# Performance work log

Hardware: AMD Instinct MI355X
Metric: run time of the kernel (lower is better)

The kernel has to match this reference:

```python
import jax, jax.numpy as jnp
import numpy as np

B, S, D, H = 4, 1024, 1024, 16
DH = D // H
K_SPARSE = 32
LAMBDA_MAX, ALPHA = 10.0, 5.0
SPARSE_THRESHOLD = 1.0


def setup_inputs() -> dict:
    key = jax.random.key(0)
    ks = jax.random.split(key, 12)
    x = jax.random.normal(ks[0], (B, S, D), dtype=jnp.float32)
    prior_mask = jax.random.bernoulli(ks[1], 0.1, (S, S))
    prior_indices = jax.random.randint(ks[2], (S, K_SPARSE), 0, S)
    prior_index_mask = jax.random.bernoulli(ks[3], 0.9, (S, K_SPARSE))
    prior_index_mask = prior_index_mask.at[:, 0].set(True)  # avoid all-masked rows
    u_prev = jax.random.normal(ks[4], (B, 1), dtype=jnp.float32)
    sc = 1.0 / np.sqrt(D)
    Wq = jax.random.normal(ks[5], (D, D), dtype=jnp.float32) * sc
    Wk = jax.random.normal(ks[6], (D, D), dtype=jnp.float32) * sc
    Wv = jax.random.normal(ks[7], (D, D), dtype=jnp.float32) * sc
    Wo = jax.random.normal(ks[8], (D, D), dtype=jnp.float32) * sc
    bq = jnp.zeros((D,), jnp.float32)
    bk = jnp.zeros((D,), jnp.float32)
    bv = jnp.zeros((D,), jnp.float32)
    bo = jnp.zeros((D,), jnp.float32)
    return {"x": x, "prior_mask": prior_mask, "prior_indices": prior_indices,
            "prior_index_mask": prior_index_mask, "u_prev": u_prev,
            "Wq": Wq, "bq": bq, "Wk": Wk, "bk": bk, "Wv": Wv, "bv": bv,
            "Wo": Wo, "bo": bo}


def reference(x, prior_mask, prior_indices, prior_index_mask, u_prev,
              Wq, bq, Wk, bk, Wv, bv, Wo, bo):
    Bb, Ss, Dd = x.shape
    scale = 1.0 / jnp.sqrt(jnp.asarray(DH, x.dtype))

    def proj(W, b):
        return (x @ W.T + b).reshape(Bb, Ss, H, DH).transpose(0, 2, 1, 3)  # [B,H,S,DH]

    Q, K, V = proj(Wq, bq), proj(Wk, bk), proj(Wv, bv)

    lam = LAMBDA_MAX * jnp.exp(-ALPHA * u_prev.reshape(Bb))  # [B]
    use_sparse = lam >= SPARSE_THRESHOLD                      # [B] bool

    # ---- dense branch: full SDPA with lambda-scaled prior bias ----
    scores = jnp.einsum('bhqd,bhkd->bhqk', Q, K) * scale      # [B,H,S,S]
    prior_bias = jnp.where(prior_mask[:Ss, :Ss], 0.0, -1.0).astype(x.dtype)
    bias = lam[:, None, None, None] * prior_bias[None, None]
    dense_out = jnp.einsum('bhqk,bhkd->bhqd',
                           jax.nn.softmax(scores + bias, axis=-1), V)

    # ---- sparse branch: gather-indexed SDPA over prior_indices ----
    idx = prior_indices[:Ss]                                   # [S,k]
    Kg = K[:, :, idx]                                          # [B,H,S,k,DH]
    Vg = V[:, :, idx]
    s_scores = jnp.einsum('bhsd,bhskd->bhsk', Q, Kg) * scale   # [B,H,S,k]
    s_scores = jnp.where(prior_index_mask[:Ss][None, None], s_scores,
                         jnp.asarray(-jnp.inf, x.dtype))
    sparse_out = jnp.einsum('bhsk,bhskd->bhsd',
                            jax.nn.softmax(s_scores, axis=-1), Vg)

    out = jnp.where(use_sparse[:, None, None, None], sparse_out, dense_out)
    out = out.transpose(0, 2, 1, 3).reshape(Bb, Ss, Dd)
    return out @ Wo.T + bo
```

## Files before the change

### kernel.cpp

```cpp
#include <hip/hip_runtime.h>
#include <hip/hip_bf16.h>
#include <cmath>

#define NB 4
#define NS 1024
#define ND 1024
#define NH 16
#define NDH 64
#define NKSP 32
#define SCALE 0.125f
#define LOG2E 1.44269504f
#define SCALE2 (SCALE * LOG2E)

typedef __attribute__((ext_vector_type(8))) short bf16x8;
typedef __attribute__((ext_vector_type(4))) float f32x4;
typedef unsigned long long u64;

#define AS1 __attribute__((address_space(1)))
#define AS3 __attribute__((address_space(3)))

__device__ __forceinline__ void gl_lds16(const void* g, void* l) {
    __builtin_amdgcn_global_load_lds((const AS1 void*)g, (AS3 void*)l, 16, 0, 0);
}

__device__ __forceinline__ ushort f2bf(float f) {
    union { __hip_bfloat16 h; ushort u; } cv;
    cv.h = __float2bfloat16(f);
    return cv.u;
}
__device__ __forceinline__ float bf2f(ushort u) {
    union { unsigned int i; float f; } cv;
    cv.i = ((unsigned int)u) << 16;
    return cv.f;
}
__device__ __forceinline__ float fexp2(float x) {
    return __builtin_amdgcn_exp2f(x);
}

__global__ __launch_bounds__(256)
void f2bf_multi(const float* __restrict__ x,
                const float* __restrict__ w0, const float* __restrict__ w1,
                const float* __restrict__ w2, const float* __restrict__ w3,
                const int* __restrict__ pm,
                ushort* __restrict__ xo,
                ushort* __restrict__ o0, ushort* __restrict__ o1,
                ushort* __restrict__ o2, ushort* __restrict__ o3,
                u64* __restrict__ bm)
{
    int y = blockIdx.y;
    if (y == 5) {
        int word = blockIdx.x * 4 + (threadIdx.x >> 6);
        int lane = threadIdx.x & 63;
        int row  = word >> 4, wcol = word & 15;
        int v = pm[(size_t)row * NS + wcol * 64 + lane];
        u64 b = __ballot(v != 0);
        if (lane == 0) bm[word] = b;
        return;
    }
    const float* src; ushort* dst; int nblk;
    if (y == 0)      { src = x;  dst = xo; nblk = 4096; }
    else if (y == 1) { src = w0; dst = o0; nblk = 1024; }
    else if (y == 2) { src = w1; dst = o1; nblk = 1024; }
    else if (y == 3) { src = w2; dst = o2; nblk = 1024; }
    else             { src = w3; dst = o3; nblk = 1024; }
    if (blockIdx.x >= (unsigned)nblk) return;
    int i = (blockIdx.x * 256 + threadIdx.x) * 4;
    float4 v = *(const float4*)&src[i];
    ushort4 o;
    o.x = f2bf(v.x); o.y = f2bf(v.y); o.z = f2bf(v.z); o.w = f2bf(v.w);
    *(ushort4*)&dst[i] = o;
}

__global__ __launch_bounds__(256)
void gemm_qkv(const ushort* __restrict__ xb,
              const ushort* __restrict__ Wqb, const ushort* __restrict__ Wkb,
              const ushort* __restrict__ Wvb,
              const float* __restrict__ bq, const float* __restrict__ bk,
              const float* __restrict__ bv,
              ushort* __restrict__ Qo, ushort* __restrict__ Ko,
              ushort* __restrict__ Vo, ushort* __restrict__ Vto)
{
    constexpr int K = ND;
    __shared__ __attribute__((aligned(16))) ushort As[128 * 32];
    __shared__ __attribute__((aligned(16))) ushort Bs[128 * 32];

    const int tid  = threadIdx.x;
    const int lane = tid & 63, w = tid >> 6;
    const int wm = w >> 1, wn = w & 1;
    const int which = blockIdx.x >> 3;
    const int n0 = (blockIdx.x & 7) * 128;
    const int m0 = blockIdx.y * 128;
    const int quad = lane >> 4, l16 = lane & 15;

    const ushort* W = (which == 0) ? Wqb : (which == 1) ? Wkb : Wvb;
    const float* bias = (which == 0) ? bq : (which == 1) ? bk : bv;
    ushort* Out = (which == 0) ? Qo : (which == 1) ? Ko : Vo;

    f32x4 acc[4][4] = {};

    for (int k0 = 0; k0 < K; k0 += 32) {
        __syncthreads();
#pragma unroll
        for (int u = 0; u < 2; ++u) {
            int t0 = u * 256 + w * 64;
            int t  = t0 + lane;
            int row = t >> 2, kc = (t & 3) * 8;
            gl_lds16(xb + (size_t)(m0 + row) * K + k0 + kc, &As[t0 * 8]);
            gl_lds16(W  + (size_t)(n0 + row) * K + k0 + kc, &Bs[t0 * 8]);
        }
        __syncthreads();

        bf16x8 af[4], bfr[4];
#pragma unroll
        for (int mt = 0; mt < 4; ++mt)
            af[mt] = *(const bf16x8*)&As[(wm*64 + mt*16 + l16) * 32 + quad*8];
#pragma unroll
        for (int nt = 0; nt < 4; ++nt)
            bfr[nt] = *(const bf16x8*)&Bs[(wn*64 + nt*16 + l16) * 32 + quad*8];
#pragma unroll
        for (int mt = 0; mt < 4; ++mt)
#pragma unroll
            for (int nt = 0; nt < 4; ++nt)
                acc[mt][nt] = __builtin_amdgcn_mfma_f32_16x16x32_bf16(
                    af[mt], bfr[nt], acc[mt][nt], 0, 0, 0);
    }

#pragma unroll
    for (int nt = 0; nt < 4; ++nt) {
        int n = n0 + wn*64 + nt*16 + l16;
        float bz = bias[n];
        int hh = n >> 6, dh = n & 63;
#pragma unroll
        for (int mt = 0; mt < 4; ++mt) {
#pragma unroll
            for (int rg = 0; rg < 4; ++rg) {
                int m = m0 + wm*64 + mt*16 + quad*4 + rg;
                int b = m >> 10, s = m & (NS - 1);
                ushort val = f2bf(acc[mt][nt][rg] + bz);
                Out[(((size_t)(b*NH + hh))*NS + s)*NDH + dh] = val;
                if (which == 2)
                    Vto[(((size_t)(b*NH + hh))*NDH + dh)*NS + s] = val;
            }
        }
    }
}

__global__ __launch_bounds__(256)
void gemm_out(const ushort* __restrict__ A, const ushort* __restrict__ W,
              const float* __restrict__ bias, float* __restrict__ Cout)
{
    constexpr int K = ND;
    __shared__ __attribute__((aligned(16))) ushort As[64 * 32];
    __shared__ __attribute__((aligned(16))) ushort Bs[128 * 32];

    const int tid  = threadIdx.x;
    const int lane = tid & 63, w = tid >> 6;
    const int wm = w & 1, wn = w >> 1;
    const int m0 = blockIdx.y * 64, n0 = blockIdx.x * 128;
    const int quad = lane >> 4, l16 = lane & 15;

    f32x4 acc[2][4] = {};

    for (int k0 = 0; k0 < K; k0 += 32) {
        __syncthreads();
        {
            int t0 = w * 64;
            int t  = t0 + lane;
            int row = t >> 2, kc = (t & 3) * 8;
            gl_lds16(A + (size_t)(m0 + row) * K + k0 + kc, &As[t0 * 8]);
        }
#pragma unroll
        for (int u = 0; u < 2; ++u) {
            int t0 = u * 256 + w * 64;
            int t  = t0 + lane;
            int row = t >> 2, kc = (t & 3) * 8;
            gl_lds16(W + (size_t)(n0 + row) * K + k0 + kc, &Bs[t0 * 8]);
        }
        __syncthreads();

        bf16x8 af[2], bfr[4];
#pragma unroll
        for (int mt = 0; mt < 2; ++mt)
            af[mt] = *(const bf16x8*)&As[(wm*32 + mt*16 + l16) * 32 + quad*8];
#pragma unroll
        for (int nt = 0; nt < 4; ++nt)
            bfr[nt] = *(const bf16x8*)&Bs[(wn*64 + nt*16 + l16) * 32 + quad*8];
#pragma unroll
        for (int mt = 0; mt < 2; ++mt)
#pragma unroll
            for (int nt = 0; nt < 4; ++nt)
                acc[mt][nt] = __builtin_amdgcn_mfma_f32_16x16x32_bf16(
                    af[mt], bfr[nt], acc[mt][nt], 0, 0, 0);
    }

#pragma unroll
    for (int nt = 0; nt < 4; ++nt) {
        int n = n0 + wn*64 + nt*16 + l16;
        float bz = bias[n];
#pragma unroll
        for (int mt = 0; mt < 2; ++mt) {
#pragma unroll
            for (int rg = 0; rg < 4; ++rg) {
                int m = m0 + wm*32 + mt*16 + quad*4 + rg;
                Cout[(size_t)m * ND + n] = acc[mt][nt][rg] + bz;
            }
        }
    }
}


#define STAGE(BUF, PT)                                                        \
    _Pragma("unroll")                                                         \
    for (int u = 0; u < 4; ++u) {                                             \
        int cb = w * 256 + u * 64;                                            \
        int c  = cb + lane;                                                   \
        int wk2 = c >> 9, c2 = c & 511;                                       \
        int row = c2 >> 3, sub = c2 & 7;                                      \
        const ushort* src = Kh + (((size_t)(((PT) + wk2)*64 + row)) << 6)     \
                               + ((sub ^ (row & 7)) << 3);                    \
        gl_lds16(src, (ushort*)KK + (BUF)*8192 + (size_t)cb * 8);             \
    }

#define LOADKV(KF, VF, BUF, KT)                                               \
    _Pragma("unroll")                                                         \
    for (int nt = 0; nt < 4; ++nt)                                            \
        _Pragma("unroll")                                                     \
        for (int kk = 0; kk < 2; ++kk) {                                      \
            int rowk = nt*16 + l16;                                           \
            int ck = (kk*4 + quad) ^ (l16 & 7);                               \
            KF[nt][kk] = *(const bf16x8*)                                     \
                &((ushort*)KK)[(BUF)*8192 + wk*4096 + rowk*64 + ck*8];        \
            VF[nt][kk] = *(const bf16x8*)                                     \
                &Vth[(size_t)(nt*16 + l16) * NS + (KT)*64 + kk*32 + quad*8];  \
        }

#define STEP(KT, KF, VF)                                                      \
    _Pragma("unroll")                                                         \
    for (int qh = 0; qh < 2; ++qh) {                                          \
        const int qrow = wq*32 + qh*16 + l16;                                 \
        u64 wqm = MW[(KT)*64 + qrow] >> (quad * 4);                           \
        f32x4 s_acc[4] = {};                                                  \
        __builtin_amdgcn_s_setprio(1);                                        \
        _Pragma("unroll")                                                     \
        for (int nt = 0; nt < 4; ++nt)                                        \
            _Pragma("unroll")                                                 \
            for (int kk = 0; kk < 2; ++kk)                                    \
                s_acc[nt] = __builtin_amdgcn_mfma_f32_16x16x32_bf16(          \
                    KF[nt][kk], qf[qh][kk], s_acc[nt], 0, 0, 0);              \
        __builtin_amdgcn_s_setprio(0);                                        \
        _Pragma("unroll")                                                     \
        for (int nt = 0; nt < 4; ++nt) {                                      \
            ushort4 pk;                                                       \
            float p0 = fexp2(fmaf(s_acc[nt][0], SCALE2,                       \
                 ((wqm >> (nt*16 + 0)) & 1ULL) ? 0.f : nlam2));               \
            float p1 = fexp2(fmaf(s_acc[nt][1], SCALE2,                       \
                 ((wqm >> (nt*16 + 1)) & 1ULL) ? 0.f : nlam2));               \
            float p2 = fexp2(fmaf(s_acc[nt][2], SCALE2,                       \
                 ((wqm >> (nt*16 + 2)) & 1ULL) ? 0.f : nlam2));               \
            float p3 = fexp2(fmaf(s_acc[nt][3], SCALE2,                       \
                 ((wqm >> (nt*16 + 3)) & 1ULL) ? 0.f : nlam2));               \
            pk.x = f2bf(p0); pk.y = f2bf(p1);                                 \
            pk.z = f2bf(p2); pk.w = f2bf(p3);                                 \
            *(ushort4*)&Ps[wk][qrow*72 + nt*16 + quad*4] = pk;                \
        }                                                                     \
        bf16x8 pf[2];                                                         \
        _Pragma("unroll")                                                     \
        for (int kk = 0; kk < 2; ++kk)                                        \
            pf[kk] = *(const bf16x8*)&Ps[wk][qrow*72 + kk*32 + quad*8];       \
        __builtin_amdgcn_s_setprio(1);                                        \
        _Pragma("unroll")                                                     \
        for (int kk = 0; kk < 2; ++kk) {                                      \
            l_acc[qh] = __builtin_amdgcn_mfma_f32_16x16x32_bf16(              \
                pf[kk], ones.v, l_acc[qh], 0, 0, 0);                          \
            _Pragma("unroll")                                                 \
            for (int nt = 0; nt < 4; ++nt)                                    \
                o_acc[qh][nt] = __builtin_amdgcn_mfma_f32_16x16x32_bf16(      \
                    pf[kk], VF[nt][kk], o_acc[qh][nt], 0, 0, 0);              \
        }                                                                     \
        __builtin_amdgcn_s_setprio(0);                                        \
    }

__global__ __launch_bounds__(256, 2)
void attn_kernel(const ushort* __restrict__ Qb, const ushort* __restrict__ Kb,
                 const ushort* __restrict__ Vb, const ushort* __restrict__ Vt,
                 const u64* __restrict__ bm,
                 const int* __restrict__ pidx, const int* __restrict__ pimask,
                 const float* __restrict__ u_prev, ushort* __restrict__ OA)
{
    __shared__ __attribute__((aligned(16))) ushort Ps[2][64 * 72];
    __shared__ __attribute__((aligned(16))) u64    MW[16 * 64];
    __shared__ __attribute__((aligned(16))) ushort KK[2][2][64 * 64];

    const int tid  = threadIdx.x;
    const int lane = tid & 63, w = tid >> 6;
    const int quad = lane >> 4, l16 = lane & 15;
    const int wq = w & 1, wk = w >> 1;

    const int id    = blockIdx.x;
    const int xcd   = id & 7;
    const int b     = ((id >> 3) + (id >> 8)) & 3;
    const int hb    = (id >> 5) & 1;
    const int qtile = (id >> 6) & 15;
    const int h     = hb * 8 + xcd;
    const int s0    = qtile * 64;

    const float lam = 10.0f * __expf(-5.0f * u_prev[b]);
    const bool sparse = (lam >= 1.0f);

    const size_t bh = (size_t)b * NH + h;
    const ushort* Qh  = Qb + bh * NS * NDH;
    const ushort* Kh  = Kb + bh * NS * NDH;
    const ushort* Vh  = Vb + bh * NS * NDH;
    const ushort* Vth = Vt + bh * NDH * NS;

    if (!sparse) {
        const float nlam2 = -lam * LOG2E;

        STAGE(0, 0);
#pragma unroll
        for (int u = 0; u < 4; ++u) {
            int idx = u * 256 + tid;
            int row = idx >> 4, wd = idx & 15;
            MW[wd * 64 + row] = bm[(size_t)s0 * 16 + idx];
        }

        bf16x8 qf[2][2];
#pragma unroll
        for (int qh = 0; qh < 2; ++qh)
#pragma unroll
            for (int kk = 0; kk < 2; ++kk)
                qf[qh][kk] = *(const bf16x8*)
                    &Qh[(size_t)(s0 + wq*32 + qh*16 + l16) * NDH + kk*32 + quad*8];

        union { bf16x8 v; ushort s[8]; } ones;
#pragma unroll
        for (int i = 0; i < 8; ++i) ones.s[i] = 0x3F80;

        f32x4 o_acc[2][4] = {};
        f32x4 l_acc[2] = {};

        __syncthreads();

        int cur = 0;
        for (int t = 0; t < 8; ++t) {
            if (t + 1 < 8) STAGE(cur ^ 1, 2*(t + 1));
            bf16x8 kf[4][2], vf[4][2];
            const int kt = 2*t + wk;
            LOADKV(kf, vf, cur, kt);
            STEP(kt, kf, vf);
            __syncthreads();
            cur ^= 1;
        }

        float* POUT = (float*)KK;
        if (wk == 1) {
#pragma unroll
            for (int qh = 0; qh < 2; ++qh) {
#pragma unroll
                for (int nt = 0; nt < 4; ++nt)
#pragma unroll
                    for (int rg = 0; rg < 4; ++rg)
                        POUT[(wq*40 + qh*16 + nt*4 + rg)*64 + lane] =
                            o_acc[qh][nt][rg];
#pragma unroll
                for (int rg = 0; rg < 4; ++rg)
                    POUT[(wq*40 + 32 + qh*4 + rg)*64 + lane] = l_acc[qh][rg];
            }
        }
        __syncthreads();
        if (wk == 0) {
#pragma unroll
            for (int qh = 0; qh < 2; ++qh) {
#pragma unroll
                for (int nt = 0; nt < 4; ++nt)
#pragma unroll
                    for (int rg = 0; rg < 4; ++rg)
                        o_acc[qh][nt][rg] +=
                            POUT[(wq*40 + qh*16 + nt*4 + rg)*64 + lane];
#pragma unroll
                for (int rg = 0; rg < 4; ++rg)
                    l_acc[qh][rg] += POUT[(wq*40 + 32 + qh*4 + rg)*64 + lane];
            }
#pragma unroll
            for (int qh = 0; qh < 2; ++qh) {
                float inv[4];
#pragma unroll
                for (int rg = 0; rg < 4; ++rg) inv[rg] = 1.f / l_acc[qh][rg];
#pragma unroll
                for (int nt = 0; nt < 4; ++nt)
#pragma unroll
                    for (int rg = 0; rg < 4; ++rg) {
                        int m = wq*32 + qh*16 + quad*4 + rg;
                        OA[((size_t)b*NS + s0 + m)*ND + h*NDH + nt*16 + l16] =
                            f2bf(o_acc[qh][nt][rg] * inv[rg]);
                    }
            }
        }
    } else {
        const int r2  = lane & 15;
        const int cg  = lane >> 4;
        {
            const int row = w*16 + r2;

            float qreg[64];
            {
                const ushort* qp = Qh + (size_t)(s0 + row) * NDH;
#pragma unroll
                for (int c = 0; c < 8; ++c) {
                    union { bf16x8 v; ushort s[8]; } qv;
                    qv.v = *(const bf16x8*)(qp + c*8);
#pragma unroll
                    for (int j = 0; j < 8; ++j) qreg[c*8 + j] = bf2f(qv.s[j]);
                }
            }

            float sc[8];
#pragma unroll
            for (int jj = 0; jj < 8; ++jj) {
                int j  = cg*8 + jj;
                int mv = pimask[(size_t)(s0+row)*NKSP + j];
                int kv = pidx[(size_t)(s0+row)*NKSP + j];
                const ushort* krow = &Kh[(size_t)kv * NDH];
                float acc = 0.f;
#pragma unroll
                for (int c = 0; c < 8; ++c) {
                    union { bf16x8 v; ushort s[8]; } kk;
                    kk.v = *(const bf16x8*)(krow + c*8);
#pragma unroll
                    for (int jb = 0; jb < 8; ++jb)
                        acc = fmaf(qreg[c*8 + jb], bf2f(kk.s[jb]), acc);
                }
                sc[jj] = mv ? acc * SCALE : -INFINITY;
            }
            float mt = sc[0];
#pragma unroll
            for (int jj = 1; jj < 8; ++jj) mt = fmaxf(mt, sc[jj]);
            mt = fmaxf(mt, __shfl_xor(mt, 16));
            mt = fmaxf(mt, __shfl_xor(mt, 32));

            float psum = 0.f;
#pragma unroll
            for (int jj = 0; jj < 8; ++jj) {
                float p = __expf(sc[jj] - mt);
                psum += p;
                Ps[0][row * 72 + cg*8 + jj] = f2bf(p);
            }
            psum += __shfl_xor(psum, 16);
            psum += __shfl_xor(psum, 32);

            float o[16];
#pragma unroll
            for (int i = 0; i < 16; ++i) o[i] = 0.f;

#pragma unroll 4
            for (int j = 0; j < 32; ++j) {
                float p = bf2f(Ps[0][row * 72 + j]);
                int kv = pidx[(size_t)(s0+row)*NKSP + j];
                const ushort* vrow = &Vh[(size_t)kv * NDH + cg*16];
#pragma unroll
                for (int c = 0; c < 2; ++c) {
                    union { bf16x8 v; ushort s[8]; } vv;
                    vv.v = *(const bf16x8*)(vrow + c*8);
#pragma unroll
                    for (int jb = 0; jb < 8; ++jb)
                        o[c*8 + jb] = fmaf(p, bf2f(vv.s[jb]), o[c*8 + jb]);
                }
            }

            float inv = 1.f / psum;
            ushort* op = OA + ((size_t)b*NS + s0 + row)*ND + h*NDH + cg*16;
#pragma unroll
            for (int i4 = 0; i4 < 4; ++i4) {
                ushort4 v;
                v.x = f2bf(o[i4*4+0]*inv); v.y = f2bf(o[i4*4+1]*inv);
                v.z = f2bf(o[i4*4+2]*inv); v.w = f2bf(o[i4*4+3]*inv);
                *(ushort4*)(op + i4*4) = v;
            }
        }
    }
}

extern "C" void kernel_launch(void* const* d_in, const int* in_sizes, int n_in,
                              void* d_out, int out_size, void* d_ws, size_t ws_size,
                              hipStream_t stream)
{
    const float* x      = (const float*)d_in[0];
    const int*   pmask  = (const int*)  d_in[1];
    const int*   pidx   = (const int*)  d_in[2];
    const int*   pimask = (const int*)  d_in[3];
    const float* u_prev = (const float*)d_in[4];
    const float* Wq     = (const float*)d_in[5];
    const float* bq     = (const float*)d_in[6];
    const float* Wk     = (const float*)d_in[7];
    const float* bk     = (const float*)d_in[8];
    const float* Wv     = (const float*)d_in[9];
    const float* bv     = (const float*)d_in[10];
    const float* Wo     = (const float*)d_in[11];
    const float* bo     = (const float*)d_in[12];
    float* out = (float*)d_out;

    const size_t QSZ = (size_t)NB * NH * NS * NDH;
    const size_t WSZ = (size_t)ND * ND;
    ushort* xb  = (ushort*)d_ws;
    ushort* Qw  = xb  + QSZ;
    ushort* Kw  = Qw  + QSZ;
    ushort* Vw  = Kw  + QSZ;
    ushort* Vtw = Vw  + QSZ;
    ushort* Awb = Vtw + QSZ;
    ushort* Wqb = Awb + QSZ;
    ushort* Wkb = Wqb + WSZ;
    ushort* Wvb = Wkb + WSZ;
    ushort* Wob = Wvb + WSZ;
    u64*    bmw = (u64*)(Wob + WSZ);

    f2bf_multi<<<dim3(4096, 6), 256, 0, stream>>>(
        x, Wq, Wk, Wv, Wo, pmask, xb, Wqb, Wkb, Wvb, Wob, bmw);

    gemm_qkv<<<dim3(24, 32), 256, 0, stream>>>(
        xb, Wqb, Wkb, Wvb, bq, bk, bv, Qw, Kw, Vw, Vtw);

    attn_kernel<<<1024, 256, 0, stream>>>(
        Qw, Kw, Vw, Vtw, bmw, pidx, pimask, u_prev, Awb);

    gemm_out<<<dim3(ND/128, (NB*NS)/64), 256, 0, stream>>>(Awb, Wob, bo, out);
}
```

Measured before the change: 226.0 us.

## Single-buffer K tiles to cut LDS, raise occupancy, regroup blocks by branch

The K staging buffer drops from double to single buffering. The mask-word LDS table is removed in favour of direct per-thread global loads of the mask bits. This shrinks shared memory enough to raise launch bounds from 2 to 4 blocks per CU. Block-to-(batch, head, tile) mapping is recomputed so dense-branch and sparse-branch batches are packed into contiguous block ranges. The trade is that each K tile now waits behind a barrier with no prefetch overlap, in exchange for more resident waves hiding latency.

```diff
diff --git a/kernel.cpp b/kernel.cpp
--- a/kernel.cpp
+++ b/kernel.cpp
@@ -209,7 +209,7 @@
 }
 
 
-#define STAGE(BUF, PT)                                                        \
+#define STAGE(PT)                                                             \
     _Pragma("unroll")                                                         \
     for (int u = 0; u < 4; ++u) {                                             \
         int cb = w * 256 + u * 64;                                            \
@@ -218,27 +218,26 @@
         int row = c2 >> 3, sub = c2 & 7;                                      \
         const ushort* src = Kh + (((size_t)(((PT) + wk2)*64 + row)) << 6)     \
                                + ((sub ^ (row & 7)) << 3);                    \
-        gl_lds16(src, (ushort*)KK + (BUF)*8192 + (size_t)cb * 8);             \
-    }
-
-#define LOADKV(KF, VF, BUF, KT)                                               \
+        gl_lds16(src, KK + (size_t)cb * 8);                                   \
+    }
+
+#define LOADKV(KF, VF, KT)                                                    \
     _Pragma("unroll")                                                         \
     for (int nt = 0; nt < 4; ++nt)                                            \
         _Pragma("unroll")                                                     \
         for (int kk = 0; kk < 2; ++kk) {                                      \
             int rowk = nt*16 + l16;                                           \
             int ck = (kk*4 + quad) ^ (l16 & 7);                               \
-            KF[nt][kk] = *(const bf16x8*)                                     \
-                &((ushort*)KK)[(BUF)*8192 + wk*4096 + rowk*64 + ck*8];        \
+            KF[nt][kk] = *(const bf16x8*)&KK[wk*4096 + rowk*64 + ck*8];       \
             VF[nt][kk] = *(const bf16x8*)                                     \
                 &Vth[(size_t)(nt*16 + l16) * NS + (KT)*64 + kk*32 + quad*8];  \
         }
 
-#define STEP(KT, KF, VF)                                                      \
+#define STEP(KF, VF, M0, M1)                                                  \
     _Pragma("unroll")                                                         \
     for (int qh = 0; qh < 2; ++qh) {                                          \
         const int qrow = wq*32 + qh*16 + l16;                                 \
-        u64 wqm = MW[(KT)*64 + qrow] >> (quad * 4);                           \
+        u64 wqm = ((qh == 0) ? (M0) : (M1)) >> (quad * 4);                    \
         f32x4 s_acc[4] = {};                                                  \
         __builtin_amdgcn_s_setprio(1);                                        \
         _Pragma("unroll")                                                     \
@@ -261,12 +260,12 @@
                  ((wqm >> (nt*16 + 3)) & 1ULL) ? 0.f : nlam2));               \
             pk.x = f2bf(p0); pk.y = f2bf(p1);                                 \
             pk.z = f2bf(p2); pk.w = f2bf(p3);                                 \
-            *(ushort4*)&Ps[wk][qrow*72 + nt*16 + quad*4] = pk;                \
+            *(ushort4*)&Ps[wk*4608 + qrow*72 + nt*16 + quad*4] = pk;          \
         }                                                                     \
         bf16x8 pf[2];                                                         \
         _Pragma("unroll")                                                     \
         for (int kk = 0; kk < 2; ++kk)                                        \
-            pf[kk] = *(const bf16x8*)&Ps[wk][qrow*72 + kk*32 + quad*8];       \
+            pf[kk] = *(const bf16x8*)&Ps[wk*4608 + qrow*72 + kk*32 + quad*8]; \
         __builtin_amdgcn_s_setprio(1);                                        \
         _Pragma("unroll")                                                     \
         for (int kk = 0; kk < 2; ++kk) {                                      \
@@ -280,32 +279,51 @@
         __builtin_amdgcn_s_setprio(0);                                        \
     }
 
-__global__ __launch_bounds__(256, 2)
+__global__ __launch_bounds__(256, 4)
 void attn_kernel(const ushort* __restrict__ Qb, const ushort* __restrict__ Kb,
                  const ushort* __restrict__ Vb, const ushort* __restrict__ Vt,
                  const u64* __restrict__ bm,
                  const int* __restrict__ pidx, const int* __restrict__ pimask,
                  const float* __restrict__ u_prev, ushort* __restrict__ OA)
 {
-    __shared__ __attribute__((aligned(16))) ushort Ps[2][64 * 72];
-    __shared__ __attribute__((aligned(16))) u64    MW[16 * 64];
-    __shared__ __attribute__((aligned(16))) ushort KK[2][2][64 * 64];
+    __shared__ __attribute__((aligned(16))) ushort SM[17408];
+    ushort* KK = SM;
+    ushort* Ps = SM + 8192;
 
     const int tid  = threadIdx.x;
     const int lane = tid & 63, w = tid >> 6;
     const int quad = lane >> 4, l16 = lane & 15;
     const int wq = w & 1, wk = w >> 1;
 
-    const int id    = blockIdx.x;
-    const int xcd   = id & 7;
-    const int b     = ((id >> 3) + (id >> 8)) & 3;
-    const int hb    = (id >> 5) & 1;
-    const int qtile = (id >> 6) & 15;
-    const int h     = hb * 8 + xcd;
-    const int s0    = qtile * 64;
-
-    const float lam = 10.0f * __expf(-5.0f * u_prev[b]);
-    const bool sparse = (lam >= 1.0f);
+    float lams[4];
+#pragma unroll
+    for (int i = 0; i < 4; ++i) lams[i] = 10.0f * __expf(-5.0f * u_prev[i]);
+    int dl[4], sl[4], nd = 0, ns = 0;
+#pragma unroll
+    for (int i = 0; i < 4; ++i) if (lams[i] <  1.0f) dl[nd++] = i;
+#pragma unroll
+    for (int i = 0; i < 4; ++i) if (lams[i] >= 1.0f) sl[ns++] = i;
+
+    const int id = blockIdx.x;
+    bool sparse; int b, h, qtile;
+    if (id < nd * 256) {
+        sparse = false;
+        int xcd = id & 7, j = id >> 3;
+        int nh2 = 2 * nd;
+        int hi = j % nh2, qt = j / nh2;
+        int gh = hi * 8 + xcd;
+        b = dl[gh >> 4]; h = gh & 15; qtile = qt;
+    } else {
+        sparse = true;
+        int d = id - nd * 256;
+        int xcd = d & 7, j = d >> 3;
+        int nh2 = 2 * ns;
+        int hi = j % nh2, qt = j / nh2;
+        int gh = hi * 8 + xcd;
+        b = sl[gh >> 4]; h = gh & 15; qtile = qt;
+    }
+    const int s0 = qtile * 64;
+    const float lam = lams[b];
 
     const size_t bh = (size_t)b * NH + h;
     const ushort* Qh  = Qb + bh * NS * NDH;
@@ -316,14 +334,6 @@
     if (!sparse) {
         const float nlam2 = -lam * LOG2E;
 
-        STAGE(0, 0);
-#pragma unroll
-        for (int u = 0; u < 4; ++u) {
-            int idx = u * 256 + tid;
-            int row = idx >> 4, wd = idx & 15;
-            MW[wd * 64 + row] = bm[(size_t)s0 * 16 + idx];
-        }
-
         bf16x8 qf[2][2];
 #pragma unroll
         for (int qh = 0; qh < 2; ++qh)
@@ -339,20 +349,20 @@
         f32x4 o_acc[2][4] = {};
         f32x4 l_acc[2] = {};
 
+        for (int t = 0; t < 8; ++t) {
+            if (t) __syncthreads();
+            STAGE(2 * t);
+            const int kt = 2 * t + wk;
+            u64 m0 = bm[(size_t)(s0 + wq*32 +  0 + l16) * 16 + kt];
+            u64 m1 = bm[(size_t)(s0 + wq*32 + 16 + l16) * 16 + kt];
+            __syncthreads();
+            bf16x8 kf[4][2], vf[4][2];
+            LOADKV(kf, vf, kt);
+            STEP(kf, vf, m0, m1);
+        }
         __syncthreads();
 
-        int cur = 0;
-        for (int t = 0; t < 8; ++t) {
-            if (t + 1 < 8) STAGE(cur ^ 1, 2*(t + 1));
-            bf16x8 kf[4][2], vf[4][2];
-            const int kt = 2*t + wk;
-            LOADKV(kf, vf, cur, kt);
-            STEP(kt, kf, vf);
-            __syncthreads();
-            cur ^= 1;
-        }
-
-        float* POUT = (float*)KK;
+        float* POUT = (float*)SM;
         if (wk == 1) {
 #pragma unroll
             for (int qh = 0; qh < 2; ++qh) {
@@ -443,7 +453,7 @@
             for (int jj = 0; jj < 8; ++jj) {
                 float p = __expf(sc[jj] - mt);
                 psum += p;
-                Ps[0][row * 72 + cg*8 + jj] = f2bf(p);
+                Ps[row * 72 + cg*8 + jj] = f2bf(p);
             }
             psum += __shfl_xor(psum, 16);
             psum += __shfl_xor(psum, 32);
@@ -454,7 +464,7 @@
 
 #pragma unroll 4
             for (int j = 0; j < 32; ++j) {
-                float p = bf2f(Ps[0][row * 72 + j]);
+                float p = bf2f(Ps[row * 72 + j]);
                 int kv = pidx[(size_t)(s0+row)*NKSP + j];
                 const ushort* vrow = &Vh[(size_t)kv * NDH + cg*16];
 #pragma unroll
```

Result: slower. 263.1 us (+16.4%).
